# Kernel tuning notes

Measured on AMD Instinct MI355X. Metric: run time of the kernel, lower is better.

Reference implementation:

```python
import jax, jax.numpy as jnp
import numpy as np

N_USERS = 100000
N_ITEMS = 100000
D = 128
L = 200
B = 4096
TAU = 4.0          # softmax temperature
BETA = 0.25        # KL weight
SIG_Q = 0.1        # hyper_approx: posterior lognormal sigma
SIG_P = 1.0        # hyper_prior: prior lognormal sigma
LN_EPS = 1e-5


def _layernorm(x, g, b):
    m = x.mean(-1, keepdims=True)
    v = ((x - m) ** 2).mean(-1, keepdims=True)
    return (x - m) / jnp.sqrt(v + LN_EPS) * g + b


def _bam(Q, K, V, mask, Wq, Wk, b_att, v_att, key):
    """Bayesian Attention Module (lognormal sampler, concat score).
    Q: (B,D), K/V: (B,L,D), mask: (B,L) bool (True = valid).
    Returns context (B,D) and scalar KL."""
    # additive / concat score: v^T tanh(Wq q + Wk k + b)
    h = jnp.tanh((Q @ Wq)[:, None, :] + jnp.einsum('bld,de->ble', K, Wk) + b_att)
    s = jnp.einsum('bld,d->bl', h, v_att) / TAU
    logits = jnp.where(mask, s, jnp.asarray(-1e9, s.dtype))
    alpha = jax.nn.softmax(logits, axis=-1)                  # (B,L)
    mu = jnp.log(alpha + 1e-24)                              # lognormal posterior mean (log-space)
    eps = jax.random.normal(key, s.shape, s.dtype)
    w = jnp.where(mask, jnp.exp(mu + SIG_Q * eps), 0.0)      # sampled unnormalized weights
    Wn = w / (w.sum(-1, keepdims=True) + 1e-12)
    ctx = jnp.einsum('bl,bld->bd', Wn, V)
    # KL(lognormal(mu, SIG_Q) || lognormal(log(1/n_valid), SIG_P)) over valid slots
    n_valid = jnp.maximum(mask.sum(-1, keepdims=True), 1).astype(s.dtype)
    mu_p = -jnp.log(n_valid)
    kl_el = np.log(SIG_P / SIG_Q) + (SIG_Q ** 2 + (mu - mu_p) ** 2) / (2.0 * SIG_P ** 2) - 0.5
    kl = BETA * jnp.where(mask, kl_el, 0.0).sum() / jnp.maximum(mask.sum(), 1).astype(s.dtype)
    return ctx, kl


def setup_inputs() -> dict:
    key = jax.random.key(0)
    ks = jax.random.split(key, 8)
    return {
        'user_emb': jax.random.normal(ks[0], (N_USERS + 1, D), jnp.float32) * 0.01,
        'item_emb': jax.random.normal(ks[1], (N_ITEMS + 1, D), jnp.float32) * 0.01,
        'Wq': jax.random.normal(ks[2], (D, D), jnp.float32) / np.sqrt(D),
        'Wk': jax.random.normal(ks[3], (D, D), jnp.float32) / np.sqrt(D),
        'b_att': jnp.zeros((D,), jnp.float32),
        'v_att': jax.random.normal(ks[4], (D,), jnp.float32) / np.sqrt(D),
        'ln_u_g': jnp.ones((D,), jnp.float32),
        'ln_u_b': jnp.zeros((D,), jnp.float32),
        'ln_i_g': jnp.ones((D,), jnp.float32),
        'ln_i_b': jnp.zeros((D,), jnp.float32),
        'pred_W': jax.random.normal(ks[5], (D, 1), jnp.float32) / np.sqrt(D),
        'pred_b': jnp.zeros((1,), jnp.float32),
        'user_hist': jax.random.randint(ks[6], (N_USERS, L), 0, N_ITEMS + 1, jnp.int32),
        'user_idx': jax.random.randint(ks[7], (B,), 0, N_USERS, jnp.int32),
        'item_idx': jax.random.randint(jax.random.fold_in(key, 7), (B,), 0, N_ITEMS, jnp.int32),
    }


def reference(user_emb, item_emb, Wq, Wk, b_att, v_att, ln_u_g, ln_u_b,
              ln_i_g, ln_i_b, pred_W, pred_b, user_hist, user_idx, item_idx):
    refer = user_hist[user_idx]                               # (B,L) item ids
    mask = (refer != item_idx[:, None]) & (refer != N_ITEMS)  # drop target item + padding
    Q = user_emb[user_idx]                                    # (B,D)
    KV = item_emb[refer]                                      # (B,L,D)
    # NOTE: original forward calls user_hist_embed_generator (bam_u) for BOTH
    # user and item history slices; replicated faithfully (two stochastic draws).
    ctx_u, kl_u = _bam(Q, KV, KV, mask, Wq, Wk, b_att, v_att, jax.random.key(1))
    ctx_i, kl_i = _bam(Q, KV, KV, mask, Wq, Wk, b_att, v_att, jax.random.key(2))
    u_slice = _layernorm(ctx_u * user_emb[user_idx], ln_u_g, ln_u_b)
    i_slice = _layernorm(ctx_i * item_emb[item_idx], ln_i_g, ln_i_b)
    pred_vec = u_slice * i_slice                              # GMF elementwise fuse
    logit = (pred_vec @ pred_W + pred_b).squeeze(-1)          # (B,)
    return logit, (kl_u + kl_i) / 2.0
```

## Files before the change

kernel.cpp:

```cpp
#include <hip/hip_runtime.h>
#include <hip/hip_bf16.h>
#include <math.h>

#define D 128
#define L 200
#define BATCH 4096
#define N_ITEMS 100000
#define NI1 (N_ITEMS + 1)
#define KWBLOCKS 782
#define QWBLOCKS 32
#define HALF_CNT (BATCH * L / 2)
#define TAU_INV 0.25f
#define SIG_Q 0.1f
#define C_KL 1.8075850929940455f
#define C_DEC 1.03845937e34f

typedef __attribute__((ext_vector_type(8))) short short8;
typedef __attribute__((ext_vector_type(4))) float float4v;
typedef __attribute__((ext_vector_type(2))) float f32x2;

#if defined(__has_builtin)
#if __has_builtin(__builtin_amdgcn_cvt_pk_f32_fp8) && __has_builtin(__builtin_amdgcn_cvt_pk_fp8_f32)
#define HWFP8 1
#endif
#endif
#ifndef HWFP8
#define HWFP8 0
#endif

__device__ __forceinline__ unsigned short f2bf(float f) {
    unsigned x = __float_as_uint(f);
    unsigned r = (x + 0x7fffu + ((x >> 16) & 1u)) >> 16;
    return (unsigned short)r;
}
__device__ __forceinline__ unsigned f2fp8(float x) {
    unsigned s = (__float_as_uint(x) >> 31) << 7;
    float ay = fabsf(x);
    unsigned b;
    if (ay < 0.015625f) {
        b = (unsigned)__float2int_rn(ay * 512.0f);
    } else {
        unsigned u = __float_as_uint(ay);
        u += 0x7ffffu + ((u >> 20) & 1u);
        unsigned e = (u >> 23) - 120u;
        b = (e << 3) | ((u >> 20) & 7u);
    }
    return b | s;
}

__device__ __forceinline__ unsigned pack4fp8(float a, float b, float c, float d) {
#if HWFP8
    int r = __builtin_amdgcn_cvt_pk_fp8_f32(a, b, 0, false);
    r = __builtin_amdgcn_cvt_pk_fp8_f32(c, d, r, true);
    return (unsigned)r;
#else
    return f2fp8(a) | (f2fp8(b) << 8) | (f2fp8(c) << 16) | (f2fp8(d) << 24);
#endif
}

#if HWFP8
__device__ __forceinline__ void dec4p(unsigned x, f32x2& lo, f32x2& hi) {
    lo = __builtin_amdgcn_cvt_pk_f32_fp8(x, false);
    hi = __builtin_amdgcn_cvt_pk_f32_fp8(x, true);
}
#else
__device__ __forceinline__ void dec4p(unsigned x, f32x2& lo, f32x2& hi) {
    const float S = C_DEC * 128.f;
    lo.x = __uint_as_float(((x & 0x80u) << 24) | ((x & 0x7fu) << 20)) * S;
    lo.y = __uint_as_float(((x & 0x8000u) << 16) | ((x & 0x7f00u) << 12)) * S;
    hi.x = __uint_as_float(((x & 0x800000u) << 8) | ((x & 0x7f0000u) << 4)) * S;
    hi.y = __uint_as_float((x & 0x80000000u) | ((x & 0x7f000000u) >> 4)) * S;
}
#endif

__device__ __forceinline__ f32x2 pfma(f32x2 a, f32x2 b, f32x2 c) {
    return __builtin_elementwise_fma(a, b, c);
}

#define DPP_ADD(x, ctrl)                                                     \
    ((x) + __uint_as_float((unsigned)__builtin_amdgcn_update_dpp(            \
               0, (int)__float_as_uint(x), ctrl, 0xF, 0xF, true)))
__device__ __forceinline__ float red32(float x) {
    x = DPP_ADD(x, 0xB1);
    x = DPP_ADD(x, 0x4E);
    x = DPP_ADD(x, 0x141);
    x = DPP_ADD(x, 0x140);
    x += __uint_as_float((unsigned)__builtin_amdgcn_ds_swizzle(
        (int)__float_as_uint(x), 0x401F));
    return x;
}

__device__ __forceinline__ unsigned rotl32(unsigned x, int r) {
    return (x << r) | (x >> (32 - r));
}

__device__ __forceinline__ void threefry2x32(unsigned k0, unsigned k1,
                                             unsigned x0, unsigned x1,
                                             unsigned& o0, unsigned& o1) {
    unsigned k2 = k0 ^ k1 ^ 0x1BD11BDAu;
    x0 += k0; x1 += k1;
#define TF_ROUND(r) { x0 += x1; x1 = rotl32(x1, r); x1 ^= x0; }
    TF_ROUND(13) TF_ROUND(15) TF_ROUND(26) TF_ROUND(6)
    x0 += k1; x1 += k2 + 1u;
    TF_ROUND(17) TF_ROUND(29) TF_ROUND(16) TF_ROUND(24)
    x0 += k2; x1 += k0 + 2u;
    TF_ROUND(13) TF_ROUND(15) TF_ROUND(26) TF_ROUND(6)
    x0 += k0; x1 += k1 + 3u;
    TF_ROUND(17) TF_ROUND(29) TF_ROUND(16) TF_ROUND(24)
    x0 += k1; x1 += k2 + 4u;
    TF_ROUND(13) TF_ROUND(15) TF_ROUND(26) TF_ROUND(6)
    x0 += k2; x1 += k0 + 5u;
#undef TF_ROUND
    o0 = x0; o1 = x1;
}

__device__ float erfinv_f32(float x) {
    float w = -log1pf(-x * x);
    float p;
    if (w < 5.0f) {
        w -= 2.5f;
        p = 2.81022636e-08f;
        p = fmaf(p, w, 3.43273939e-07f);
        p = fmaf(p, w, -3.5233877e-06f);
        p = fmaf(p, w, -4.39150654e-06f);
        p = fmaf(p, w, 0.00021858087f);
        p = fmaf(p, w, -0.00125372503f);
        p = fmaf(p, w, -0.00417768164f);
        p = fmaf(p, w, 0.246640727f);
        p = fmaf(p, w, 1.50140941f);
    } else {
        w = sqrtf(w) - 3.0f;
        p = -0.000200214257f;
        p = fmaf(p, w, 0.000100950558f);
        p = fmaf(p, w, 0.00134934322f);
        p = fmaf(p, w, -0.00367342844f);
        p = fmaf(p, w, 0.00573950773f);
        p = fmaf(p, w, -0.0076224613f);
        p = fmaf(p, w, 0.00943887047f);
        p = fmaf(p, w, 1.00167406f);
        p = fmaf(p, w, 2.83297682f);
    }
    return p * x;
}

__device__ float bits_to_normal(unsigned bits) {
    float f = __uint_as_float((bits >> 9) | 0x3f800000u) - 1.0f;
    const float mn = -0.99999994f;
    float scale = 1.0f - mn;
    float u = fmaf(f, scale, mn);
    u = fmaxf(mn, u);
    return 1.4142135623730951f * erfinv_f32(u);
}

__global__ __launch_bounds__(128) void wk_prep(const float* __restrict__ Wk,
                                               const float* __restrict__ Wq,
                                               unsigned short* __restrict__ WkTb,
                                               unsigned short* __restrict__ WqTb,
                                               float* __restrict__ accum) {
    int n = blockIdx.x & 127;
    const float* src = (blockIdx.x < 128) ? Wk : Wq;
    unsigned short* dst = (blockIdx.x < 128) ? WkTb : WqTb;
    int k = threadIdx.x;
    dst[n * D + k] = f2bf(src[k * D + n]);
    if (blockIdx.x == 0 && k == 0) {
        accum[0] = 0.f;
        ((unsigned*)accum)[1] = 0u;
    }
}

__global__ __launch_bounds__(256) void tables_kernel(
    const float* __restrict__ item_emb, const float* __restrict__ user_emb,
    const int* __restrict__ user_idx,
    const unsigned short* __restrict__ WkTb, const unsigned short* __restrict__ WqTb,
    const float* __restrict__ b_att,
    unsigned char* __restrict__ PT, float* __restrict__ qW) {
    __shared__ unsigned char stage[128 * 256];
    int t = threadIdx.x;
    int w = t >> 6, lane = t & 63;
    int lq = lane >> 4, lm = lane & 15;
    int bx = blockIdx.x;

    if (bx < KWBLOCKS) {
        int r0 = bx * 128;
        int rw = w * 32;
        short8 afr[2][4];
#pragma unroll
        for (int tm = 0; tm < 2; tm++) {
            int rowl = rw + tm * 16 + lm;
            int row = r0 + rowl;
            bool ok = row < NI1;
            const float* src = item_emb + (size_t)row * D;
            unsigned sbase = rowl * 256;
            int rsw = rowl & 15;
#pragma unroll
            for (int kc = 0; kc < 4; kc++) {
                float4 a = ok ? *(const float4*)(src + kc * 32 + lq * 8)
                              : make_float4(0.f, 0.f, 0.f, 0.f);
                float4 c = ok ? *(const float4*)(src + kc * 32 + lq * 8 + 4)
                              : make_float4(0.f, 0.f, 0.f, 0.f);
                short8 f;
                f[0] = (short)f2bf(a.x); f[1] = (short)f2bf(a.y);
                f[2] = (short)f2bf(a.z); f[3] = (short)f2bf(a.w);
                f[4] = (short)f2bf(c.x); f[5] = (short)f2bf(c.y);
                f[6] = (short)f2bf(c.z); f[7] = (short)f2bf(c.w);
                afr[tm][kc] = f;
                int u = kc * 4 + lq;
                unsigned* dst = (unsigned*)(stage + sbase + ((unsigned)(u ^ rsw) << 4));
                dst[1] = pack4fp8(a.x * 128.f, a.y * 128.f, a.z * 128.f, a.w * 128.f);
                dst[3] = pack4fp8(c.x * 128.f, c.y * 128.f, c.z * 128.f, c.w * 128.f);
            }
        }
        float4v acc[2][8];
#pragma unroll
        for (int tm = 0; tm < 2; tm++)
#pragma unroll
            for (int tn = 0; tn < 8; tn++) acc[tm][tn] = (float4v)(0.f);
#pragma unroll
        for (int tn = 0; tn < 8; tn++) {
#pragma unroll
            for (int kc = 0; kc < 4; kc++) {
                short8 bfr = *(const short8*)(WkTb + (tn * 16 + lm) * D + kc * 32 + lq * 8);
                acc[0][tn] = __builtin_amdgcn_mfma_f32_16x16x32_bf16(bfr, afr[0][kc], acc[0][tn], 0, 0, 0);
                acc[1][tn] = __builtin_amdgcn_mfma_f32_16x16x32_bf16(bfr, afr[1][kc], acc[1][tn], 0, 0, 0);
            }
        }
#pragma unroll
        for (int tm = 0; tm < 2; tm++) {
            int rowl = rw + tm * 16 + lm;
            int rsw = rowl & 15;
            unsigned sbase = rowl * 256;
#pragma unroll
            for (int tn = 0; tn < 8; tn++) {
                unsigned dw = pack4fp8(acc[tm][tn][0] * 128.f, acc[tm][tn][1] * 128.f,
                                       acc[tm][tn][2] * 128.f, acc[tm][tn][3] * 128.f);
                int cc = 4 * tn + lq;
                int u = cc >> 1;
                *(unsigned*)(stage + sbase + ((unsigned)(u ^ rsw) << 4) +
                             ((unsigned)(cc & 1) << 3)) = dw;
            }
        }
        __syncthreads();
#pragma unroll
        for (int i = 0; i < 8; i++) {
            int gidx = i * 256 + t;
            int rowl = gidx >> 4, u = gidx & 15;
            int row = r0 + rowl;
            if (row < NI1) {
                float4 vv = *(const float4*)(stage + rowl * 256 +
                                             ((unsigned)(u ^ (rowl & 15)) << 4));
                *(float4*)(PT + (size_t)row * 256 + (unsigned)u * 16) = vv;
            }
        }
    } else {
        int r0 = (bx - KWBLOCKS) * 128 + w * 32;
        int urow0 = user_idx[r0 + lm];
        int urow1 = user_idx[r0 + 16 + lm];
        short8 afr[2][4];
#pragma unroll
        for (int tm = 0; tm < 2; tm++) {
            const float* src = user_emb + (size_t)(tm ? urow1 : urow0) * D;
#pragma unroll
            for (int kc = 0; kc < 4; kc++) {
                float4 a = *(const float4*)(src + kc * 32 + lq * 8);
                float4 c = *(const float4*)(src + kc * 32 + lq * 8 + 4);
                short8 f;
                f[0] = (short)f2bf(a.x); f[1] = (short)f2bf(a.y);
                f[2] = (short)f2bf(a.z); f[3] = (short)f2bf(a.w);
                f[4] = (short)f2bf(c.x); f[5] = (short)f2bf(c.y);
                f[6] = (short)f2bf(c.z); f[7] = (short)f2bf(c.w);
                afr[tm][kc] = f;
            }
        }
        float4v acc[2][8];
#pragma unroll
        for (int tm = 0; tm < 2; tm++)
#pragma unroll
            for (int tn = 0; tn < 8; tn++) acc[tm][tn] = (float4v)(0.f);
#pragma unroll
        for (int tn = 0; tn < 8; tn++) {
#pragma unroll
            for (int kc = 0; kc < 4; kc++) {
                short8 bfr = *(const short8*)(WqTb + (tn * 16 + lm) * D + kc * 32 + lq * 8);
                acc[0][tn] = __builtin_amdgcn_mfma_f32_16x16x32_bf16(afr[0][kc], bfr, acc[0][tn], 0, 0, 0);
                acc[1][tn] = __builtin_amdgcn_mfma_f32_16x16x32_bf16(afr[1][kc], bfr, acc[1][tn], 0, 0, 0);
            }
        }
#pragma unroll
        for (int tm = 0; tm < 2; tm++)
#pragma unroll
            for (int tn = 0; tn < 8; tn++) {
                float bv = b_att[tn * 16 + lm];
#pragma unroll
                for (int i = 0; i < 4; i++) {
                    int row = r0 + tm * 16 + lq * 4 + i;
                    qW[(size_t)row * D + tn * 16 + lm] = acc[tm][tn][i] + bv;
                }
            }
    }
}

#define TC3 (-1.2270929e-14f)
#define TC2 (4.9670537e-10f)
#define TC1 (-2.0345052e-5f)

__global__ __launch_bounds__(256) void fused_kernel(
    const unsigned char* __restrict__ PT, const float* __restrict__ qW,
    const float* __restrict__ v_att,
    const float* __restrict__ user_emb, const float* __restrict__ item_emb,
    const int* __restrict__ user_hist, const int* __restrict__ user_idx,
    const int* __restrict__ item_idx,
    const float* __restrict__ ln_u_g, const float* __restrict__ ln_u_b,
    const float* __restrict__ ln_i_g, const float* __restrict__ ln_i_b,
    const float* __restrict__ pred_W, const float* __restrict__ pred_b,
    float* __restrict__ out, float* __restrict__ kl_sum,
    unsigned int* __restrict__ kl_cnt) {
    int b = blockIdx.x;
    int t = threadIdx.x;
    int g = t >> 5, ln5 = t & 31, w_ = t >> 6, lane = t & 63;
    __shared__ int refer[L];
    __shared__ float2 r12[L];
    __shared__ float4 gsA[8];
    __shared__ float2 gsB[8];
    __shared__ float paccU[8][D], paccI[8][D];
    __shared__ float us_s[D];
    __shared__ float wredA[4], wredB[4], wredC[4];

    int u = user_idx[b], tgt = item_idx[b];
    if (t < L) refer[t] = user_hist[(size_t)u * L + t];

    float4 q4 = *(const float4*)(qW + (size_t)b * D + ln5 * 4);
    float4 v4 = *(const float4*)(v_att + ln5 * 4);
    f32x2 qA = {q4.x * 128.f, q4.y * 128.f};
    f32x2 qB = {q4.z * 128.f, q4.w * 128.f};
    const float VS = TAU_INV / 128.f;
    f32x2 vAs = {v4.x * VS, v4.y * VS};
    f32x2 vBs = {v4.z * VS, v4.w * VS};

    __syncthreads();

    int l0 = g * 25;
    uint2 kvb[2][5];
    unsigned lnoff = (unsigned)(ln5 * 8);
#pragma unroll
    for (int c0 = 0; c0 < 2; c0++) {
#pragma unroll
        for (int j = 0; j < 5; j++) {
            unsigned it = (unsigned)refer[l0 + c0 * 5 + j];
            kvb[c0][j] = *(const uint2*)(PT + ((it << 8) | lnoff));
        }
    }

    if (t < L) {
        int f = b * L + t;
        unsigned o0, o1, bits1, bits2;
        if (f < HALF_CNT) {
            threefry2x32(0u, 1u, (unsigned)f, (unsigned)(f + HALF_CNT), o0, o1);
            bits1 = o0;
            threefry2x32(0u, 2u, (unsigned)f, (unsigned)(f + HALF_CNT), o0, o1);
            bits2 = o0;
        } else {
            threefry2x32(0u, 1u, (unsigned)(f - HALF_CNT), (unsigned)f, o0, o1);
            bits1 = o1;
            threefry2x32(0u, 2u, (unsigned)(f - HALF_CNT), (unsigned)f, o0, o1);
            bits2 = o1;
        }
        r12[t] = make_float2(__expf(SIG_Q * bits_to_normal(bits1)),
                             __expf(SIG_Q * bits_to_normal(bits2)));
    }
    __syncthreads();

    f32x2 aU01 = {0.f, 0.f}, aU23 = {0.f, 0.f};
    f32x2 aI01 = {0.f, 0.f}, aI23 = {0.f, 0.f};
    float se = 0.f, sw1 = 0.f, sw2 = 0.f, ss = 0.f, ss2 = 0.f, cn = 0.f;
    const f32x2 tc3v = {TC3, TC3}, tc2v = {TC2, TC2}, tc1v = {TC1, TC1};
    const f32x2 onev = {1.f, 1.f};
#pragma unroll
    for (int c = 0; c < 5; c++) {
        const int cur = c & 1;
#pragma unroll
        for (int j = 0; j < 5; j++) {
            unsigned kx = kvb[cur][j].x, ky = kvb[cur][j].y;
            f32x2 kA, kB;
            dec4p(kx, kA, kB);
            f32x2 xA = kA + qA, xB = kB + qB;
            f32x2 x2A = xA * xA, x2B = xB * xB;
            f32x2 pA = pfma(x2A, tc3v, tc2v);
            f32x2 pB = pfma(x2B, tc3v, tc2v);
            pA = pfma(x2A, pA, tc1v);
            pB = pfma(x2B, pB, tc1v);
            pA = pfma(x2A, pA, onev);
            pB = pfma(x2B, pB, onev);
            f32x2 pr = (xA * pA) * vAs;
            pr = pfma(xB * pB, vBs, pr);
            float s = red32(pr.x + pr.y);
            int it = refer[l0 + c * 5 + j];
            bool valid = (it != tgt) && (it != N_ITEMS);
            float e = valid ? __expf(s) : 0.f;
            float sm = valid ? s : 0.f;
            se += e; ss += sm; ss2 = fmaf(sm, sm, ss2);
            cn += valid ? 1.f : 0.f;
            float2 r = r12[l0 + c * 5 + j];
            float ed = e * 0.0078125f;
            float w1 = ed * r.x, w2 = ed * r.y;
            sw1 += w1; sw2 += w2;
            f32x2 vvA, vvB;
            dec4p(ky, vvA, vvB);
            f32x2 w1v = {w1, w1}, w2v = {w2, w2};
            aU01 = pfma(w1v, vvA, aU01); aU23 = pfma(w1v, vvB, aU23);
            aI01 = pfma(w2v, vvA, aI01); aI23 = pfma(w2v, vvB, aI23);
        }
        if (c < 3) {
#pragma unroll
            for (int j = 0; j < 5; j++) {
                unsigned it = (unsigned)refer[l0 + (c + 2) * 5 + j];
                kvb[cur][j] = *(const uint2*)(PT + ((it << 8) | lnoff));
            }
        }
    }
    if (ln5 == 0) {
        gsA[g] = make_float4(se, sw1, sw2, cn);
        gsB[g] = make_float2(ss, ss2);
    }
    *(float4*)&paccU[g][ln5 * 4] = make_float4(aU01.x, aU01.y, aU23.x, aU23.y);
    *(float4*)&paccI[g][ln5 * 4] = make_float4(aI01.x, aI01.y, aI23.x, aI23.y);
    __syncthreads();

    float sum_e = 0.f, sum_w1 = 0.f, sum_w2 = 0.f, cntf = 0.f, ssum = 0.f, ss2um = 0.f;
#pragma unroll
    for (int g2 = 0; g2 < 8; g2++) {
        float4 a = gsA[g2]; float2 c = gsB[g2];
        sum_e += a.x; sum_w1 += a.y; sum_w2 += a.z; cntf += a.w;
        ssum += c.x; ss2um += c.y;
    }
    int n_valid_raw = (int)(cntf + 0.5f);
    int n_valid = n_valid_raw < 1 ? 1 : n_valid_raw;
    float T = __logf(sum_e + 1e-30f) - __logf((float)n_valid);
    float klb = cntf * C_KL +
                0.5f * (ss2um - 2.f * T * ssum + cntf * T * T);
    float inv1 = 0.0078125f / (sum_w1 + 1e-14f);
    float inv2 = 0.0078125f / (sum_w2 + 1e-14f);

    int d = t & 127, half = t >> 7;
    float ctx = 0.f;
    if (half) {
#pragma unroll
        for (int g2 = 0; g2 < 8; g2++) ctx += paccI[g2][d];
        ctx *= inv2;
    } else {
#pragma unroll
        for (int g2 = 0; g2 < 8; g2++) ctx += paccU[g2][d];
        ctx *= inv1;
    }
    float own = ctx * (half ? item_emb[(size_t)tgt * D + d]
                            : user_emb[(size_t)u * D + d]);
    float rsum = own;
#pragma unroll
    for (int m = 1; m < 64; m <<= 1) rsum += __shfl_xor(rsum, m);
    if (lane == 0) wredA[w_] = rsum;
    __syncthreads();
    float mean = (wredA[half * 2] + wredA[half * 2 + 1]) * (1.f / 128.f);
    float dv = own - mean;
    float vsum = dv * dv;
#pragma unroll
    for (int m = 1; m < 64; m <<= 1) vsum += __shfl_xor(vsum, m);
    if (lane == 0) wredB[w_] = vsum;
    __syncthreads();
    float var = (wredB[half * 2] + wredB[half * 2 + 1]) * (1.f / 128.f);
    float gg = half ? ln_i_g[d] : ln_u_g[d];
    float bb = half ? ln_i_b[d] : ln_u_b[d];
    float sl = dv * rsqrtf(var + 1e-5f) * gg + bb;
    if (!half) us_s[d] = sl;
    __syncthreads();
    float contrib = half ? (us_s[d] * sl * pred_W[d]) : 0.f;
#pragma unroll
    for (int m = 1; m < 64; m <<= 1) contrib += __shfl_xor(contrib, m);
    if (lane == 0) wredC[w_] = contrib;
    __syncthreads();
    if (t == 0) {
        out[b] = wredC[2] + wredC[3] + pred_b[0];
        atomicAdd(kl_sum, klb);
        atomicAdd(kl_cnt, (unsigned)n_valid_raw);
    }
}

__global__ void finalize_kernel(const float* __restrict__ kl_sum,
                                const unsigned int* __restrict__ kl_cnt,
                                float* __restrict__ out_kl) {
    unsigned c = *kl_cnt;
    if (c < 1u) c = 1u;
    *out_kl = 0.25f * (*kl_sum) / (float)c;
}

extern "C" void kernel_launch(void* const* d_in, const int* in_sizes, int n_in,
                              void* d_out, int out_size, void* d_ws, size_t ws_size,
                              hipStream_t stream) {
    (void)in_sizes; (void)n_in; (void)out_size; (void)ws_size;
    const float* user_emb = (const float*)d_in[0];
    const float* item_emb = (const float*)d_in[1];
    const float* Wq       = (const float*)d_in[2];
    const float* Wk       = (const float*)d_in[3];
    const float* b_att    = (const float*)d_in[4];
    const float* v_att    = (const float*)d_in[5];
    const float* ln_u_g   = (const float*)d_in[6];
    const float* ln_u_b   = (const float*)d_in[7];
    const float* ln_i_g   = (const float*)d_in[8];
    const float* ln_i_b   = (const float*)d_in[9];
    const float* pred_W   = (const float*)d_in[10];
    const float* pred_b   = (const float*)d_in[11];
    const int* user_hist  = (const int*)d_in[12];
    const int* user_idx   = (const int*)d_in[13];
    const int* item_idx   = (const int*)d_in[14];
    float* out = (float*)d_out;

    unsigned char* PT = (unsigned char*)d_ws;
    float* qW    = (float*)(PT + (size_t)NI1 * 256);
    float* accum = qW + (size_t)BATCH * D;
    unsigned short* WkTb = (unsigned short*)(accum + 4);
    unsigned short* WqTb = WkTb + D * D;

    wk_prep<<<256, 128, 0, stream>>>(Wk, Wq, WkTb, WqTb, accum);
    tables_kernel<<<KWBLOCKS + QWBLOCKS, 256, 0, stream>>>(
        item_emb, user_emb, user_idx, WkTb, WqTb, b_att, PT, qW);
    fused_kernel<<<BATCH, 256, 0, stream>>>(PT, qW, v_att, user_emb,
                                            item_emb, user_hist, user_idx,
                                            item_idx, ln_u_g, ln_u_b, ln_i_g,
                                            ln_i_b, pred_W, pred_b, out, accum,
                                            (unsigned int*)(accum + 1));
    finalize_kernel<<<1, 1, 0, stream>>>(accum, (const unsigned int*)(accum + 1),
                                         out + BATCH);
}
```

Measured before the change: 333.1 us.

## Process two batch elements per block and replace KL atomics with partial sums

The fused kernel now handles two batch elements per 256-thread block. Each group of 32 lanes covers 50 history rows of one element instead of 25 rows of a single element, and the launch uses half as many blocks. The per-block KL sum and count atomics are replaced by per-block partial arrays that a 256-thread finalize kernel reduces, so the accumulator reset in wk_prep is dropped. The aim is to amortise per-block setup and RNG overhead and remove global atomic contention. The cost is that the LayerNorm epilogue runs serially twice per block with more barriers, and the count is now accumulated in float.

```diff
diff --git a/kernel.cpp b/kernel.cpp
--- a/kernel.cpp
+++ b/kernel.cpp
@@ -5,6 +5,8 @@
 #define D 128
 #define L 200
 #define BATCH 4096
+#define EPB 2
+#define NBLK (BATCH / EPB)
 #define N_ITEMS 100000
 #define NI1 (N_ITEMS + 1)
 #define KWBLOCKS 782
@@ -155,17 +157,12 @@
 __global__ __launch_bounds__(128) void wk_prep(const float* __restrict__ Wk,
                                                const float* __restrict__ Wq,
                                                unsigned short* __restrict__ WkTb,
-                                               unsigned short* __restrict__ WqTb,
-                                               float* __restrict__ accum) {
+                                               unsigned short* __restrict__ WqTb) {
     int n = blockIdx.x & 127;
     const float* src = (blockIdx.x < 128) ? Wk : Wq;
     unsigned short* dst = (blockIdx.x < 128) ? WkTb : WqTb;
     int k = threadIdx.x;
     dst[n * D + k] = f2bf(src[k * D + n]);
-    if (blockIdx.x == 0 && k == 0) {
-        accum[0] = 0.f;
-        ((unsigned*)accum)[1] = 0u;
-    }
 }
 
 __global__ __launch_bounds__(256) void tables_kernel(
@@ -312,23 +309,30 @@
     const float* __restrict__ ln_u_g, const float* __restrict__ ln_u_b,
     const float* __restrict__ ln_i_g, const float* __restrict__ ln_i_b,
     const float* __restrict__ pred_W, const float* __restrict__ pred_b,
-    float* __restrict__ out, float* __restrict__ kl_sum,
-    unsigned int* __restrict__ kl_cnt) {
-    int b = blockIdx.x;
+    float* __restrict__ out, float* __restrict__ kl_part,
+    float* __restrict__ cnt_part) {
+    int b2 = blockIdx.x;
     int t = threadIdx.x;
     int g = t >> 5, ln5 = t & 31, w_ = t >> 6, lane = t & 63;
-    __shared__ int refer[L];
-    __shared__ float2 r12[L];
+    int e = g >> 2, gi = g & 3;
+    __shared__ int refer[EPB * L];
+    __shared__ float2 r12[EPB * L];
     __shared__ float4 gsA[8];
     __shared__ float2 gsB[8];
     __shared__ float paccU[8][D], paccI[8][D];
     __shared__ float us_s[D];
     __shared__ float wredA[4], wredB[4], wredC[4];
 
-    int u = user_idx[b], tgt = item_idx[b];
-    if (t < L) refer[t] = user_hist[(size_t)u * L + t];
-
-    float4 q4 = *(const float4*)(qW + (size_t)b * D + ln5 * 4);
+    int u0 = user_idx[2 * b2], u1 = user_idx[2 * b2 + 1];
+    int tgt0 = item_idx[2 * b2], tgt1 = item_idx[2 * b2 + 1];
+    for (int i = t; i < EPB * L; i += 256) {
+        int el = (i >= L);
+        refer[i] = user_hist[(size_t)(el ? u1 : u0) * L + (i - el * L)];
+    }
+
+    int be = 2 * b2 + e;
+    int tgt = e ? tgt1 : tgt0;
+    float4 q4 = *(const float4*)(qW + (size_t)be * D + ln5 * 4);
     float4 v4 = *(const float4*)(v_att + ln5 * 4);
     f32x2 qA = {q4.x * 128.f, q4.y * 128.f};
     f32x2 qB = {q4.z * 128.f, q4.w * 128.f};
@@ -338,20 +342,22 @@
 
     __syncthreads();
 
-    int l0 = g * 25;
-    uint2 kvb[2][5];
+    int l0r = e * L + gi * 50;
+    uint2 kv0[5], kv1[5];
     unsigned lnoff = (unsigned)(ln5 * 8);
 #pragma unroll
-    for (int c0 = 0; c0 < 2; c0++) {
-#pragma unroll
-        for (int j = 0; j < 5; j++) {
-            unsigned it = (unsigned)refer[l0 + c0 * 5 + j];
-            kvb[c0][j] = *(const uint2*)(PT + ((it << 8) | lnoff));
-        }
-    }
-
-    if (t < L) {
-        int f = b * L + t;
+    for (int j = 0; j < 5; j++) {
+        unsigned it = (unsigned)refer[l0r + j];
+        kv0[j] = *(const uint2*)(PT + ((it << 8) | lnoff));
+    }
+#pragma unroll
+    for (int j = 0; j < 5; j++) {
+        unsigned it = (unsigned)refer[l0r + 5 + j];
+        kv1[j] = *(const uint2*)(PT + ((it << 8) | lnoff));
+    }
+
+    for (int i = t; i < EPB * L; i += 256) {
+        int f = b2 * (EPB * L) + i;
         unsigned o0, o1, bits1, bits2;
         if (f < HALF_CNT) {
             threefry2x32(0u, 1u, (unsigned)f, (unsigned)(f + HALF_CNT), o0, o1);
@@ -364,7 +370,7 @@
             threefry2x32(0u, 2u, (unsigned)(f - HALF_CNT), (unsigned)f, o0, o1);
             bits2 = o1;
         }
-        r12[t] = make_float2(__expf(SIG_Q * bits_to_normal(bits1)),
+        r12[i] = make_float2(__expf(SIG_Q * bits_to_normal(bits1)),
                              __expf(SIG_Q * bits_to_normal(bits2)));
     }
     __syncthreads();
@@ -374,49 +380,58 @@
     float se = 0.f, sw1 = 0.f, sw2 = 0.f, ss = 0.f, ss2 = 0.f, cn = 0.f;
     const f32x2 tc3v = {TC3, TC3}, tc2v = {TC2, TC2}, tc1v = {TC1, TC1};
     const f32x2 onev = {1.f, 1.f};
-#pragma unroll
-    for (int c = 0; c < 5; c++) {
-        const int cur = c & 1;
-#pragma unroll
-        for (int j = 0; j < 5; j++) {
-            unsigned kx = kvb[cur][j].x, ky = kvb[cur][j].y;
-            f32x2 kA, kB;
-            dec4p(kx, kA, kB);
-            f32x2 xA = kA + qA, xB = kB + qB;
-            f32x2 x2A = xA * xA, x2B = xB * xB;
-            f32x2 pA = pfma(x2A, tc3v, tc2v);
-            f32x2 pB = pfma(x2B, tc3v, tc2v);
-            pA = pfma(x2A, pA, tc1v);
-            pB = pfma(x2B, pB, tc1v);
-            pA = pfma(x2A, pA, onev);
-            pB = pfma(x2B, pB, onev);
-            f32x2 pr = (xA * pA) * vAs;
-            pr = pfma(xB * pB, vBs, pr);
-            float s = red32(pr.x + pr.y);
-            int it = refer[l0 + c * 5 + j];
-            bool valid = (it != tgt) && (it != N_ITEMS);
-            float e = valid ? __expf(s) : 0.f;
-            float sm = valid ? s : 0.f;
-            se += e; ss += sm; ss2 = fmaf(sm, sm, ss2);
-            cn += valid ? 1.f : 0.f;
-            float2 r = r12[l0 + c * 5 + j];
-            float ed = e * 0.0078125f;
-            float w1 = ed * r.x, w2 = ed * r.y;
-            sw1 += w1; sw2 += w2;
-            f32x2 vvA, vvB;
-            dec4p(ky, vvA, vvB);
-            f32x2 w1v = {w1, w1}, w2v = {w2, w2};
-            aU01 = pfma(w1v, vvA, aU01); aU23 = pfma(w1v, vvB, aU23);
-            aI01 = pfma(w2v, vvA, aI01); aI23 = pfma(w2v, vvB, aI23);
-        }
-        if (c < 3) {
-#pragma unroll
-            for (int j = 0; j < 5; j++) {
-                unsigned it = (unsigned)refer[l0 + (c + 2) * 5 + j];
-                kvb[cur][j] = *(const uint2*)(PT + ((it << 8) | lnoff));
-            }
-        }
-    }
+
+#define ROWS5(KV, CC)                                                         \
+    _Pragma("unroll")                                                         \
+    for (int j = 0; j < 5; j++) {                                             \
+        int li = l0r + (CC) * 5 + j;                                          \
+        unsigned kx = KV[j].x, ky = KV[j].y;                                  \
+        f32x2 kA, kB;                                                         \
+        dec4p(kx, kA, kB);                                                    \
+        f32x2 xA = kA + qA, xB = kB + qB;                                     \
+        f32x2 x2A = xA * xA, x2B = xB * xB;                                   \
+        f32x2 pA = pfma(x2A, tc3v, tc2v);                                     \
+        f32x2 pB = pfma(x2B, tc3v, tc2v);                                     \
+        pA = pfma(x2A, pA, tc1v);                                             \
+        pB = pfma(x2B, pB, tc1v);                                             \
+        pA = pfma(x2A, pA, onev);                                             \
+        pB = pfma(x2B, pB, onev);                                             \
+        f32x2 pr = (xA * pA) * vAs;                                           \
+        pr = pfma(xB * pB, vBs, pr);                                          \
+        float s = red32(pr.x + pr.y);                                         \
+        int it = refer[li];                                                   \
+        bool valid = (it != tgt) && (it != N_ITEMS);                          \
+        float ev = valid ? __expf(s) : 0.f;                                   \
+        float sm = valid ? s : 0.f;                                           \
+        se += ev; ss += sm; ss2 = fmaf(sm, sm, ss2);                          \
+        cn += valid ? 1.f : 0.f;                                              \
+        float2 r = r12[li];                                                   \
+        float ed = ev * 0.0078125f;                                           \
+        float w1 = ed * r.x, w2 = ed * r.y;                                   \
+        sw1 += w1; sw2 += w2;                                                 \
+        f32x2 vvA, vvB;                                                       \
+        dec4p(ky, vvA, vvB);                                                  \
+        f32x2 w1v = {w1, w1}, w2v = {w2, w2};                                 \
+        aU01 = pfma(w1v, vvA, aU01); aU23 = pfma(w1v, vvB, aU23);             \
+        aI01 = pfma(w2v, vvA, aI01); aI23 = pfma(w2v, vvB, aI23);             \
+    }
+#define PREF5(KV, CC)                                                         \
+    _Pragma("unroll")                                                         \
+    for (int j = 0; j < 5; j++) {                                             \
+        unsigned it = (unsigned)refer[l0r + (CC) * 5 + j];                    \
+        KV[j] = *(const uint2*)(PT + ((it << 8) | lnoff));                    \
+    }
+
+    for (int ph = 0; ph < 5; ph++) {
+        int ca = 2 * ph;
+        ROWS5(kv0, ca)
+        if (ph < 4) { PREF5(kv0, ca + 2) }
+        ROWS5(kv1, ca + 1)
+        if (ph < 4) { PREF5(kv1, ca + 3) }
+    }
+#undef ROWS5
+#undef PREF5
+
     if (ln5 == 0) {
         gsA[g] = make_float4(se, sw1, sw2, cn);
         gsB[g] = make_float2(ss, ss2);
@@ -425,70 +440,90 @@
     *(float4*)&paccI[g][ln5 * 4] = make_float4(aI01.x, aI01.y, aI23.x, aI23.y);
     __syncthreads();
 
-    float sum_e = 0.f, sum_w1 = 0.f, sum_w2 = 0.f, cntf = 0.f, ssum = 0.f, ss2um = 0.f;
-#pragma unroll
-    for (int g2 = 0; g2 < 8; g2++) {
-        float4 a = gsA[g2]; float2 c = gsB[g2];
-        sum_e += a.x; sum_w1 += a.y; sum_w2 += a.z; cntf += a.w;
-        ssum += c.x; ss2um += c.y;
-    }
-    int n_valid_raw = (int)(cntf + 0.5f);
-    int n_valid = n_valid_raw < 1 ? 1 : n_valid_raw;
-    float T = __logf(sum_e + 1e-30f) - __logf((float)n_valid);
-    float klb = cntf * C_KL +
-                0.5f * (ss2um - 2.f * T * ssum + cntf * T * T);
-    float inv1 = 0.0078125f / (sum_w1 + 1e-14f);
-    float inv2 = 0.0078125f / (sum_w2 + 1e-14f);
-
+    float klb_tot = 0.f, cnt_tot = 0.f;
     int d = t & 127, half = t >> 7;
-    float ctx = 0.f;
-    if (half) {
-#pragma unroll
-        for (int g2 = 0; g2 < 8; g2++) ctx += paccI[g2][d];
-        ctx *= inv2;
-    } else {
-#pragma unroll
-        for (int g2 = 0; g2 < 8; g2++) ctx += paccU[g2][d];
-        ctx *= inv1;
-    }
-    float own = ctx * (half ? item_emb[(size_t)tgt * D + d]
-                            : user_emb[(size_t)u * D + d]);
-    float rsum = own;
-#pragma unroll
-    for (int m = 1; m < 64; m <<= 1) rsum += __shfl_xor(rsum, m);
-    if (lane == 0) wredA[w_] = rsum;
-    __syncthreads();
-    float mean = (wredA[half * 2] + wredA[half * 2 + 1]) * (1.f / 128.f);
-    float dv = own - mean;
-    float vsum = dv * dv;
-#pragma unroll
-    for (int m = 1; m < 64; m <<= 1) vsum += __shfl_xor(vsum, m);
-    if (lane == 0) wredB[w_] = vsum;
-    __syncthreads();
-    float var = (wredB[half * 2] + wredB[half * 2 + 1]) * (1.f / 128.f);
-    float gg = half ? ln_i_g[d] : ln_u_g[d];
-    float bb = half ? ln_i_b[d] : ln_u_b[d];
-    float sl = dv * rsqrtf(var + 1e-5f) * gg + bb;
-    if (!half) us_s[d] = sl;
-    __syncthreads();
-    float contrib = half ? (us_s[d] * sl * pred_W[d]) : 0.f;
-#pragma unroll
-    for (int m = 1; m < 64; m <<= 1) contrib += __shfl_xor(contrib, m);
-    if (lane == 0) wredC[w_] = contrib;
+#pragma unroll
+    for (int e2 = 0; e2 < 2; e2++) {
+        float sum_e = 0.f, sum_w1 = 0.f, sum_w2 = 0.f, cntf = 0.f, ssum = 0.f, ss2um = 0.f;
+#pragma unroll
+        for (int g2 = 0; g2 < 4; g2++) {
+            float4 a = gsA[e2 * 4 + g2]; float2 c = gsB[e2 * 4 + g2];
+            sum_e += a.x; sum_w1 += a.y; sum_w2 += a.z; cntf += a.w;
+            ssum += c.x; ss2um += c.y;
+        }
+        int n_valid_raw = (int)(cntf + 0.5f);
+        int n_valid = n_valid_raw < 1 ? 1 : n_valid_raw;
+        float T = __logf(sum_e + 1e-30f) - __logf((float)n_valid);
+        klb_tot += cntf * C_KL + 0.5f * (ss2um - 2.f * T * ssum + cntf * T * T);
+        cnt_tot += cntf;
+        float inv1 = 0.0078125f / (sum_w1 + 1e-14f);
+        float inv2 = 0.0078125f / (sum_w2 + 1e-14f);
+
+        float ctx = 0.f;
+        if (half) {
+#pragma unroll
+            for (int g2 = 0; g2 < 4; g2++) ctx += paccI[e2 * 4 + g2][d];
+            ctx *= inv2;
+        } else {
+#pragma unroll
+            for (int g2 = 0; g2 < 4; g2++) ctx += paccU[e2 * 4 + g2][d];
+            ctx *= inv1;
+        }
+        int ue = e2 ? u1 : u0, te = e2 ? tgt1 : tgt0;
+        float own = ctx * (half ? item_emb[(size_t)te * D + d]
+                                : user_emb[(size_t)ue * D + d]);
+        float rsum = own;
+#pragma unroll
+        for (int m = 1; m < 64; m <<= 1) rsum += __shfl_xor(rsum, m);
+        if (lane == 0) wredA[w_] = rsum;
+        __syncthreads();
+        float mean = (wredA[half * 2] + wredA[half * 2 + 1]) * (1.f / 128.f);
+        float dv = own - mean;
+        float vsum = dv * dv;
+#pragma unroll
+        for (int m = 1; m < 64; m <<= 1) vsum += __shfl_xor(vsum, m);
+        if (lane == 0) wredB[w_] = vsum;
+        __syncthreads();
+        float var = (wredB[half * 2] + wredB[half * 2 + 1]) * (1.f / 128.f);
+        float gg = half ? ln_i_g[d] : ln_u_g[d];
+        float bb = half ? ln_i_b[d] : ln_u_b[d];
+        float sl = dv * rsqrtf(var + 1e-5f) * gg + bb;
+        if (!half) us_s[d] = sl;
+        __syncthreads();
+        float contrib = half ? (us_s[d] * sl * pred_W[d]) : 0.f;
+#pragma unroll
+        for (int m = 1; m < 64; m <<= 1) contrib += __shfl_xor(contrib, m);
+        if (lane == 0) wredC[w_] = contrib;
+        __syncthreads();
+        if (t == 0) out[2 * b2 + e2] = wredC[2] + wredC[3] + pred_b[0];
+    }
+    if (t == 0) {
+        kl_part[b2] = klb_tot;
+        cnt_part[b2] = cnt_tot;
+    }
+}
+
+__global__ __launch_bounds__(256) void finalize_kernel(
+    const float* __restrict__ kl_part, const float* __restrict__ cnt_part,
+    float* __restrict__ out_kl) {
+    int t = threadIdx.x;
+    float s = 0.f, c = 0.f;
+    for (int i = t; i < NBLK; i += 256) { s += kl_part[i]; c += cnt_part[i]; }
+#pragma unroll
+    for (int m = 1; m < 64; m <<= 1) {
+        s += __shfl_xor(s, m);
+        c += __shfl_xor(c, m);
+    }
+    __shared__ float sh[8];
+    int w = t >> 6, lane = t & 63;
+    if (lane == 0) { sh[w * 2] = s; sh[w * 2 + 1] = c; }
     __syncthreads();
     if (t == 0) {
-        out[b] = wredC[2] + wredC[3] + pred_b[0];
-        atomicAdd(kl_sum, klb);
-        atomicAdd(kl_cnt, (unsigned)n_valid_raw);
-    }
-}
-
-__global__ void finalize_kernel(const float* __restrict__ kl_sum,
-                                const unsigned int* __restrict__ kl_cnt,
-                                float* __restrict__ out_kl) {
-    unsigned c = *kl_cnt;
-    if (c < 1u) c = 1u;
-    *out_kl = 0.25f * (*kl_sum) / (float)c;
+        float S = sh[0] + sh[2] + sh[4] + sh[6];
+        float C = sh[1] + sh[3] + sh[5] + sh[7];
+        if (C < 1.f) C = 1.f;
+        *out_kl = 0.25f * S / C;
+    }
 }
 
 extern "C" void kernel_launch(void* const* d_in, const int* in_sizes, int n_in,
@@ -513,19 +548,19 @@
     float* out = (float*)d_out;
 
     unsigned char* PT = (unsigned char*)d_ws;
-    float* qW    = (float*)(PT + (size_t)NI1 * 256);
-    float* accum = qW + (size_t)BATCH * D;
-    unsigned short* WkTb = (unsigned short*)(accum + 4);
+    float* qW      = (float*)(PT + (size_t)NI1 * 256);
+    float* kl_part = qW + (size_t)BATCH * D;
+    float* cnt_part = kl_part + NBLK;
+    unsigned short* WkTb = (unsigned short*)(cnt_part + NBLK);
     unsigned short* WqTb = WkTb + D * D;
 
-    wk_prep<<<256, 128, 0, stream>>>(Wk, Wq, WkTb, WqTb, accum);
+    wk_prep<<<256, 128, 0, stream>>>(Wk, Wq, WkTb, WqTb);
     tables_kernel<<<KWBLOCKS + QWBLOCKS, 256, 0, stream>>>(
         item_emb, user_emb, user_idx, WkTb, WqTb, b_att, PT, qW);
-    fused_kernel<<<BATCH, 256, 0, stream>>>(PT, qW, v_att, user_emb,
-                                            item_emb, user_hist, user_idx,
-                                            item_idx, ln_u_g, ln_u_b, ln_i_g,
-                                            ln_i_b, pred_W, pred_b, out, accum,
-                                            (unsigned int*)(accum + 1));
-    finalize_kernel<<<1, 1, 0, stream>>>(accum, (const unsigned int*)(accum + 1),
-                                         out + BATCH);
-}
+    fused_kernel<<<NBLK, 256, 0, stream>>>(PT, qW, v_att, user_emb,
+                                           item_emb, user_hist, user_idx,
+                                           item_idx, ln_u_g, ln_u_b, ln_i_g,
+                                           ln_i_b, pred_W, pred_b, out, kl_part,
+                                           cnt_part);
+    finalize_kernel<<<1, 256, 0, stream>>>(kl_part, cnt_part, out + BATCH);
+}
```

New measurement: 268.5 us. 19.4% less time.
